# Kernel optimization log

Hardware: AMD Instinct MI355X
Metric: run time of the kernel (lower is better)

## Reference

```python
import jax, jax.numpy as jnp
import numpy as np

B, T, V, H, M = 32, 40, 64, 768, 64
U = 23            # number of never-visited vpids
N = 63            # total distinct vpids: visited 0..T-1, unvisited T..N-1
POS_D = 7         # angle_feat_size(4) + 3
MAX_STEPS = 100
TXT_L = 60
LN_EPS = 1e-12


def setup_inputs() -> dict:
    key = jax.random.key(0)
    ks = jax.random.split(key, 12)
    split_traj_embeds = jax.random.normal(ks[0], (B, T, V, H), jnp.float32)
    split_traj_vp_lens = jax.random.randint(ks[1], (B, T), 1, V + 1)
    traj_vpids = jnp.broadcast_to(jnp.arange(T, dtype=jnp.int32), (B, T))
    cand = jax.random.randint(ks[2], (B, T, V), 0, N).astype(jnp.int32)
    # guarantee every unvisited vpid (T..N-1) appears as a candidate at step 0
    cand = cand.at[:, 0, :U].set(jnp.broadcast_to(T + jnp.arange(U, dtype=jnp.int32), (B, U)))
    # gmap node 0 is the 'stop' token (feature forced to zero); nodes 1.. list all vpids
    gmap_vpids = jnp.broadcast_to(
        jnp.concatenate([jnp.zeros((1,), jnp.int32), jnp.arange(N, dtype=jnp.int32)]), (B, M))
    gmap_step_ids = jax.random.randint(ks[3], (B, M), 0, MAX_STEPS).astype(jnp.int32)
    gmap_pos_fts = jax.random.normal(ks[4], (B, M, POS_D), jnp.float32)
    gmap_lens = jax.random.randint(ks[5], (B,), M // 2, M + 1).astype(jnp.int32)
    txt_embeds = jax.random.normal(ks[6], (B, TXT_L, H), jnp.float32)
    txt_masks = jnp.ones((B, TXT_L), bool)
    # learned params
    W_pos = jax.random.normal(ks[7], (POS_D, H), jnp.float32) / np.sqrt(POS_D)
    b_pos = jnp.zeros((H,), jnp.float32)
    ln_gamma = jnp.ones((H,), jnp.float32)
    ln_beta = jnp.zeros((H,), jnp.float32)
    step_table = jax.random.normal(ks[8], (MAX_STEPS, H), jnp.float32) * 0.02
    return {
        'txt_embeds': txt_embeds, 'txt_masks': txt_masks,
        'split_traj_embeds': split_traj_embeds, 'split_traj_vp_lens': split_traj_vp_lens,
        'traj_vpids': traj_vpids, 'traj_cand_vpids': cand, 'gmap_vpids': gmap_vpids,
        'gmap_step_ids': gmap_step_ids, 'gmap_pos_fts': gmap_pos_fts, 'gmap_lens': gmap_lens,
        'W_pos': W_pos, 'b_pos': b_pos, 'ln_gamma': ln_gamma, 'ln_beta': ln_beta,
        'step_table': step_table,
    }


def _aggregate(split_traj_embeds, vp_lens, traj_vpids, traj_cand_vpids, gmap_vpids):
    dt = split_traj_embeds.dtype
    # mask out padded views, like split_traj_embeds * vp_masks
    view_mask = (jnp.arange(V) < vp_lens[:, :, None]).astype(dt)        # [B,T,V]
    emb_masked = split_traj_embeds * view_mask[..., None]               # [B,T,V,H]
    # per-step visited feature: sum over views / vp_len
    step_mean = emb_masked.sum(axis=2) / vp_lens[..., None].astype(dt)  # [B,T,H]
    # visited lookup: last step t with traj_vpids == gmap vpid
    visit_match = gmap_vpids[:, :, None] == traj_vpids[:, None, :]      # [B,M,T]
    visited = jnp.any(visit_match, axis=-1)                             # [B,M]
    last_t = jnp.argmax(jnp.where(visit_match, jnp.arange(T), -1), axis=-1)  # [B,M]
    visited_feat = step_mean[jnp.arange(B)[:, None], last_t]            # [B,M,H]
    # unvisited: mean of candidate-slot features over all (t, j) matches
    cand_match = (gmap_vpids[:, :, None, None] == traj_cand_vpids[:, None, :, :]).astype(dt)  # [B,M,T,V]
    unvis_sum = jnp.einsum('bmtv,btvh->bmh', cand_match, emb_masked)
    cnt = cand_match.sum(axis=(2, 3))                                   # [B,M]
    unvis_feat = unvis_sum / jnp.maximum(cnt, 1.0)[..., None]
    agg = jnp.where(visited[..., None], visited_feat, unvis_feat)       # [B,M,H]
    return agg.at[:, 0, :].set(0.0)  # stop-token slot is zeros


def _layernorm(x, gamma, beta):
    mu = x.mean(axis=-1, keepdims=True)
    var = ((x - mu) ** 2).mean(axis=-1, keepdims=True)
    return (x - mu) * jax.lax.rsqrt(var + LN_EPS) * gamma + beta


def reference(txt_embeds, txt_masks, split_traj_embeds, split_traj_vp_lens, traj_vpids,
              traj_cand_vpids, gmap_vpids, gmap_step_ids, gmap_pos_fts, gmap_lens,
              W_pos, b_pos, ln_gamma, ln_beta, step_table):
    agg = _aggregate(split_traj_embeds, split_traj_vp_lens, traj_vpids,
                     traj_cand_vpids, gmap_vpids)
    pos = _layernorm(gmap_pos_fts @ W_pos + b_pos, ln_gamma, ln_beta)   # [B,M,H]
    step = step_table[gmap_step_ids]                                    # [B,M,H]
    gmap_embeds = agg + step + pos
    return gmap_embeds
```

## Files before the change

kernel.cpp:

```cpp
#include <hip/hip_runtime.h>
#include <cstdint>

#define B 32
#define T 40
#define V 64
#define H 768
#define M 64
#define POS_D 7
#define NCODE 64
#define SEG 48
#define NBIN_BLKS (B * NCODE)
#define NSTEP (B * T)
#define NTAIL B

__device__ __forceinline__ void epilogue(
    int b, int m, float ax, float ay, float az, float aw,
    const float* __restrict__ pos_fts, const float* __restrict__ W_pos,
    const float* __restrict__ b_pos, const float* __restrict__ gamma,
    const float* __restrict__ beta, const int* __restrict__ step_ids,
    const float* __restrict__ step_tab, float* __restrict__ out,
    float* w1, float* w2)
{
    const int tid = threadIdx.x;
    const int hl = tid * 4;
    const int bm = b * M + m;

    float f[POS_D];
    #pragma unroll
    for (int d = 0; d < POS_D; ++d) f[d] = pos_fts[bm * POS_D + d];
    const float4 bp = *(const float4*)(b_pos + hl);
    float px = bp.x, py = bp.y, pz = bp.z, pw = bp.w;
    #pragma unroll
    for (int d = 0; d < POS_D; ++d) {
        const float4 wv4 = *(const float4*)(W_pos + d * H + hl);
        px += f[d] * wv4.x; py += f[d] * wv4.y;
        pz += f[d] * wv4.z; pw += f[d] * wv4.w;
    }

    float s1 = px + py + pz + pw;
    float s2 = px * px + py * py + pz * pz + pw * pw;
    #pragma unroll
    for (int off = 32; off > 0; off >>= 1) {
        s1 += __shfl_xor(s1, off);
        s2 += __shfl_xor(s2, off);
    }
    __syncthreads();
    const int wv = tid >> 6;
    if ((tid & 63) == 0) { w1[wv] = s1; w2[wv] = s2; }
    __syncthreads();
    s1 = w1[0] + w1[1] + w1[2];
    s2 = w2[0] + w2[1] + w2[2];
    const float mu = s1 * (1.0f / H);
    const float var = fmaxf(s2 * (1.0f / H) - mu * mu, 0.f);
    const float rs = rsqrtf(var + 1e-12f);

    const float4 gm = *(const float4*)(gamma + hl);
    const float4 bt4 = *(const float4*)(beta + hl);
    const int sid = step_ids[bm];
    const float4 st = *(const float4*)(step_tab + (size_t)sid * H + hl);

    float4 o;
    o.x = ax + st.x + (px - mu) * rs * gm.x + bt4.x;
    o.y = ay + st.y + (py - mu) * rs * gm.y + bt4.y;
    o.z = az + st.z + (pz - mu) * rs * gm.z + bt4.z;
    o.w = aw + st.w + (pw - mu) * rs * gm.w + bt4.w;
    *(float4*)(out + (size_t)bm * H + hl) = o;
}

__global__ __launch_bounds__(192) void fused_kernel(
    const float* __restrict__ emb, const int* __restrict__ lens,
    const int* __restrict__ cand, const int* __restrict__ tvp,
    const int* __restrict__ gvp, const int* __restrict__ step_ids,
    const float* __restrict__ pos_fts, const float* __restrict__ W_pos,
    const float* __restrict__ b_pos, const float* __restrict__ gamma,
    const float* __restrict__ beta, const float* __restrict__ step_tab,
    float* __restrict__ out)
{
    const int tid = threadIdx.x;
    const int blk = blockIdx.x;
    const int w = tid >> 6, lane = tid & 63;

    __shared__ int tvp_s[T], gvp_s[M], lens_s[T];
    __shared__ int code_s, cnt_s;
    __shared__ int list_s[3 * SEG];
    __shared__ int wcnt[3];
    __shared__ float w1[3], w2[3];

    if (blk < NBIN_BLKS) {
        const int b = blk >> 6, bin = blk & 63;

        if (tid < T) { tvp_s[tid] = tvp[b * T + tid]; lens_s[tid] = lens[b * T + tid]; }
        if (tid < M) gvp_s[tid] = gvp[b * M + tid];
        if (tid == 0) { code_s = -1; cnt_s = 0; }
        if (tid < 3) wcnt[tid] = 0;
        __syncthreads();

        if (tid < 64) {
            const int c = tid;
            bool mention = false;
            #pragma unroll 8
            for (int mm = 0; mm < M; ++mm) mention |= (gvp_s[mm] == c);
            bool vis = false;
            #pragma unroll 8
            for (int t = 0; t < T; ++t) vis |= (tvp_s[t] == c);
            const bool needed = mention && !vis;
            const unsigned long long mask = __ballot(needed);
            const int pre = __popcll(mask & ((1ull << c) - 1ull));
            if (needed && pre == bin) code_s = c;
        }
        __syncthreads();

        const int code = code_s;
        if (code < 0) return;

        const int* cb = cand + b * T * V;
        int local = 0;
        for (int i = tid; i < T * V; i += 192) local += (cb[i] == code);
        #pragma unroll
        for (int off = 32; off; off >>= 1) local += __shfl_xor(local, off);
        if (lane == 0) atomicAdd(&cnt_s, local);

        int myn = 0;
        for (int t = w; t < T; t += 3) {
            const int cc = cb[t * V + lane];
            const bool ok = (lane < lens_s[t]) && (cc == code);
            const unsigned long long mk = __ballot(ok);
            if (ok) {
                const int pos = myn + __popcll(mk & ((1ull << lane) - 1ull));
                if (pos < SEG) list_s[w * SEG + pos] = t * V + lane;
            }
            myn += __popcll(mk);
        }
        if (lane == 0) wcnt[w] = min(myn, SEG);
        __syncthreads();

        float ax = 0.f, ay = 0.f, az = 0.f, aw = 0.f;
        const float* eb = emb + (size_t)b * T * V * H + tid * 4;
        for (int ww = 0; ww < 3; ++ww) {
            const int n = wcnt[ww];
            #pragma unroll 8
            for (int k = 0; k < n; ++k) {
                const int tvx = list_s[ww * SEG + k];
                const float4 x = *(const float4*)(eb + (size_t)tvx * H);
                ax += x.x; ay += x.y; az += x.z; aw += x.w;
            }
        }
        const float inv = 1.0f / fmaxf((float)cnt_s, 1.0f);
        ax *= inv; ay *= inv; az *= inv; aw *= inv;

        for (int m = 1; m < M; ++m)
            if (gvp_s[m] == code)
                epilogue(b, m, ax, ay, az, aw, pos_fts, W_pos, b_pos,
                         gamma, beta, step_ids, step_tab, out, w1, w2);
        return;
    }

    if (blk < NBIN_BLKS + NSTEP) {
        const int bt = blk - NBIN_BLKS;
        const int b = bt / T, t = bt - b * T;

        if (tid < T) tvp_s[tid] = tvp[b * T + tid];
        if (tid < M) gvp_s[tid] = gvp[b * M + tid];
        __syncthreads();

        const int c = tvp_s[t];
        int lt = -1;
        #pragma unroll 8
        for (int tt = 0; tt < T; ++tt) if (tvp_s[tt] == c) lt = tt;
        if (lt != t) return;

        bool any = false;
        #pragma unroll 8
        for (int m = 1; m < M; ++m) any |= (gvp_s[m] == c);
        if (!any) return;

        const int len = lens[bt];
        const float* base = emb + (size_t)bt * V * H + tid * 4;
        float ax = 0.f, ay = 0.f, az = 0.f, aw = 0.f;
        int v = 0;
        for (; v + 16 <= len; v += 16) {
            #pragma unroll
            for (int u = 0; u < 16; ++u) {
                const float4 x = *(const float4*)(base + (size_t)(v + u) * H);
                ax += x.x; ay += x.y; az += x.z; aw += x.w;
            }
        }
        #pragma unroll 4
        for (; v < len; ++v) {
            const float4 x = *(const float4*)(base + (size_t)v * H);
            ax += x.x; ay += x.y; az += x.z; aw += x.w;
        }
        const float inv = 1.0f / (float)len;
        ax *= inv; ay *= inv; az *= inv; aw *= inv;

        for (int m = 1; m < M; ++m)
            if (gvp_s[m] == c)
                epilogue(b, m, ax, ay, az, aw, pos_fts, W_pos, b_pos,
                         gamma, beta, step_ids, step_tab, out, w1, w2);
        return;
    }

    {
        const int b = blk - (NBIN_BLKS + NSTEP);
        if (tid < M) gvp_s[tid] = gvp[b * M + tid];
        __syncthreads();
        for (int m = 0; m < M; ++m) {
            const int g = gvp_s[m];
            const bool handled = (m != 0) && (g >= 0) && (g < NCODE);
            if (!handled)
                epilogue(b, m, 0.f, 0.f, 0.f, 0.f, pos_fts, W_pos, b_pos,
                         gamma, beta, step_ids, step_tab, out, w1, w2);
        }
    }
}

extern "C" void kernel_launch(void* const* d_in, const int* in_sizes, int n_in,
                              void* d_out, int out_size, void* d_ws, size_t ws_size,
                              hipStream_t stream)
{
    const float* emb      = (const float*)d_in[2];
    const int*   vp_lens  = (const int*)d_in[3];
    const int*   tvp      = (const int*)d_in[4];
    const int*   cand     = (const int*)d_in[5];
    const int*   gvp      = (const int*)d_in[6];
    const int*   step_ids = (const int*)d_in[7];
    const float* pos_fts  = (const float*)d_in[8];
    const float* W_pos    = (const float*)d_in[10];
    const float* b_pos    = (const float*)d_in[11];
    const float* gamma    = (const float*)d_in[12];
    const float* beta     = (const float*)d_in[13];
    const float* step_tab = (const float*)d_in[14];
    float* out = (float*)d_out;

    fused_kernel<<<NBIN_BLKS + NSTEP + NTAIL, 192, 0, stream>>>(
        emb, vp_lens, cand, tvp, gvp, step_ids, pos_fts,
        W_pos, b_pos, gamma, beta, step_tab, out);
}
```

Before: 43.20 us.

## Double block size to split row reductions across two thread halves and reorder blocks

```diff
diff --git a/kernel.cpp b/kernel.cpp
--- a/kernel.cpp
+++ b/kernel.cpp
@@ -8,13 +8,15 @@
 #define M 64
 #define POS_D 7
 #define NCODE 64
-#define SEG 48
+#define THREADS 384
+#define SEGW 24
+#define NSTEP (B * T)
 #define NBIN_BLKS (B * NCODE)
-#define NSTEP (B * T)
 #define NTAIL B
 
 __device__ __forceinline__ void epilogue(
     int b, int m, float ax, float ay, float az, float aw,
+    bool act, int col4,
     const float* __restrict__ pos_fts, const float* __restrict__ W_pos,
     const float* __restrict__ b_pos, const float* __restrict__ gamma,
     const float* __restrict__ beta, const int* __restrict__ step_ids,
@@ -22,19 +24,22 @@
     float* w1, float* w2)
 {
     const int tid = threadIdx.x;
-    const int hl = tid * 4;
+    const int wv = tid >> 6, lane = tid & 63;
     const int bm = b * M + m;
 
-    float f[POS_D];
-    #pragma unroll
-    for (int d = 0; d < POS_D; ++d) f[d] = pos_fts[bm * POS_D + d];
-    const float4 bp = *(const float4*)(b_pos + hl);
-    float px = bp.x, py = bp.y, pz = bp.z, pw = bp.w;
-    #pragma unroll
-    for (int d = 0; d < POS_D; ++d) {
-        const float4 wv4 = *(const float4*)(W_pos + d * H + hl);
-        px += f[d] * wv4.x; py += f[d] * wv4.y;
-        pz += f[d] * wv4.z; pw += f[d] * wv4.w;
+    float px = 0.f, py = 0.f, pz = 0.f, pw = 0.f;
+    if (act) {
+        float f[POS_D];
+        #pragma unroll
+        for (int d = 0; d < POS_D; ++d) f[d] = pos_fts[bm * POS_D + d];
+        const float4 bp = *(const float4*)(b_pos + col4);
+        px = bp.x; py = bp.y; pz = bp.z; pw = bp.w;
+        #pragma unroll
+        for (int d = 0; d < POS_D; ++d) {
+            const float4 wv4 = *(const float4*)(W_pos + d * H + col4);
+            px += f[d] * wv4.x; py += f[d] * wv4.y;
+            pz += f[d] * wv4.z; pw += f[d] * wv4.w;
+        }
     }
 
     float s1 = px + py + pz + pw;
@@ -45,29 +50,29 @@
         s2 += __shfl_xor(s2, off);
     }
     __syncthreads();
-    const int wv = tid >> 6;
-    if ((tid & 63) == 0) { w1[wv] = s1; w2[wv] = s2; }
+    if (lane == 0) { w1[wv] = s1; w2[wv] = s2; }
     __syncthreads();
-    s1 = w1[0] + w1[1] + w1[2];
-    s2 = w2[0] + w2[1] + w2[2];
+    s1 = w1[0] + w1[1] + w1[2] + w1[3] + w1[4] + w1[5];
+    s2 = w2[0] + w2[1] + w2[2] + w2[3] + w2[4] + w2[5];
     const float mu = s1 * (1.0f / H);
     const float var = fmaxf(s2 * (1.0f / H) - mu * mu, 0.f);
     const float rs = rsqrtf(var + 1e-12f);
 
-    const float4 gm = *(const float4*)(gamma + hl);
-    const float4 bt4 = *(const float4*)(beta + hl);
-    const int sid = step_ids[bm];
-    const float4 st = *(const float4*)(step_tab + (size_t)sid * H + hl);
-
-    float4 o;
-    o.x = ax + st.x + (px - mu) * rs * gm.x + bt4.x;
-    o.y = ay + st.y + (py - mu) * rs * gm.y + bt4.y;
-    o.z = az + st.z + (pz - mu) * rs * gm.z + bt4.z;
-    o.w = aw + st.w + (pw - mu) * rs * gm.w + bt4.w;
-    *(float4*)(out + (size_t)bm * H + hl) = o;
+    if (act) {
+        const float4 gm = *(const float4*)(gamma + col4);
+        const float4 bt4 = *(const float4*)(beta + col4);
+        const int sid = step_ids[bm];
+        const float4 st = *(const float4*)(step_tab + (size_t)sid * H + col4);
+        float4 o;
+        o.x = ax + st.x + (px - mu) * rs * gm.x + bt4.x;
+        o.y = ay + st.y + (py - mu) * rs * gm.y + bt4.y;
+        o.z = az + st.z + (pz - mu) * rs * gm.z + bt4.z;
+        o.w = aw + st.w + (pw - mu) * rs * gm.w + bt4.w;
+        *(float4*)(out + (size_t)bm * H + col4) = o;
+    }
 }
 
-__global__ __launch_bounds__(192) void fused_kernel(
+__global__ __launch_bounds__(THREADS) void fused_kernel(
     const float* __restrict__ emb, const int* __restrict__ lens,
     const int* __restrict__ cand, const int* __restrict__ tvp,
     const int* __restrict__ gvp, const int* __restrict__ step_ids,
@@ -78,21 +83,92 @@
 {
     const int tid = threadIdx.x;
     const int blk = blockIdx.x;
-    const int w = tid >> 6, lane = tid & 63;
+    const int wv = tid >> 6, lane = tid & 63;
+    const bool act = tid < 192;
+    const int sub = act ? 0 : 1;
+    const int col4 = (act ? tid : tid - 192) * 4;
 
     __shared__ int tvp_s[T], gvp_s[M], lens_s[T];
     __shared__ int code_s, cnt_s;
-    __shared__ int list_s[3 * SEG];
-    __shared__ int wcnt[3];
-    __shared__ float w1[3], w2[3];
-
-    if (blk < NBIN_BLKS) {
-        const int b = blk >> 6, bin = blk & 63;
+    __shared__ int list_s[6 * SEGW];
+    __shared__ int wcnt[6];
+    __shared__ float comb[H];
+    __shared__ float w1[6], w2[6];
+
+    if (blk < NSTEP) {
+        const int bt = blk;
+        const int b = bt / T, t = bt - b * T;
+        if (tid < T) tvp_s[tid] = tvp[b * T + tid];
+        if (tid < M) gvp_s[tid] = gvp[b * M + tid];
+        __syncthreads();
+
+        const int c = tvp_s[t];
+        int lt = -1;
+        #pragma unroll 8
+        for (int tt = 0; tt < T; ++tt) if (tvp_s[tt] == c) lt = tt;
+        if (lt != t) return;
+        bool any = false;
+        #pragma unroll 8
+        for (int m = 1; m < M; ++m) any |= (gvp_s[m] == c);
+        if (!any) return;
+
+        const int len = lens[bt];
+        const float* base = emb + (size_t)bt * V * H + col4;
+        float ax = 0.f, ay = 0.f, az = 0.f, aw = 0.f;
+        int v = 0;
+        for (; v + 32 <= len; v += 32) {
+            #pragma unroll
+            for (int u = 0; u < 16; ++u) {
+                const float4 x = *(const float4*)(base + (size_t)(v + 2 * u + sub) * H);
+                ax += x.x; ay += x.y; az += x.z; aw += x.w;
+            }
+        }
+        for (; v + 16 <= len; v += 16) {
+            #pragma unroll
+            for (int u = 0; u < 8; ++u) {
+                const float4 x = *(const float4*)(base + (size_t)(v + 2 * u + sub) * H);
+                ax += x.x; ay += x.y; az += x.z; aw += x.w;
+            }
+        }
+        for (; v + 8 <= len; v += 8) {
+            #pragma unroll
+            for (int u = 0; u < 4; ++u) {
+                const float4 x = *(const float4*)(base + (size_t)(v + 2 * u + sub) * H);
+                ax += x.x; ay += x.y; az += x.z; aw += x.w;
+            }
+        }
+        for (; v + 2 <= len; v += 2) {
+            const float4 x = *(const float4*)(base + (size_t)(v + sub) * H);
+            ax += x.x; ay += x.y; az += x.z; aw += x.w;
+        }
+        if (v < len && sub == 0) {
+            const float4 x = *(const float4*)(base + (size_t)v * H);
+            ax += x.x; ay += x.y; az += x.z; aw += x.w;
+        }
+        if (!act) { float4 o; o.x = ax; o.y = ay; o.z = az; o.w = aw;
+                    *(float4*)(comb + col4) = o; }
+        __syncthreads();
+        if (act) {
+            const float4 o = *(const float4*)(comb + col4);
+            const float inv = 1.0f / (float)len;
+            ax = (ax + o.x) * inv; ay = (ay + o.y) * inv;
+            az = (az + o.z) * inv; aw = (aw + o.w) * inv;
+        }
+        for (int m = 1; m < M; ++m)
+            if (gvp_s[m] == c)
+                epilogue(b, m, ax, ay, az, aw, act, col4, pos_fts, W_pos, b_pos,
+                         gamma, beta, step_ids, step_tab, out, w1, w2);
+        return;
+    }
+
+    if (blk < NSTEP + NBIN_BLKS) {
+        const int bb = blk - NSTEP;
+        const int b = bb >> 6, bin = bb & 63;
 
         if (tid < T) { tvp_s[tid] = tvp[b * T + tid]; lens_s[tid] = lens[b * T + tid]; }
         if (tid < M) gvp_s[tid] = gvp[b * M + tid];
         if (tid == 0) { code_s = -1; cnt_s = 0; }
-        if (tid < 3) wcnt[tid] = 0;
+        if (tid < 6) wcnt[tid] = 0;
         __syncthreads();
 
         if (tid < 64) {
@@ -115,101 +191,61 @@
 
         const int* cb = cand + b * T * V;
         int local = 0;
-        for (int i = tid; i < T * V; i += 192) local += (cb[i] == code);
+        for (int i = tid; i < T * V; i += THREADS) local += (cb[i] == code);
         #pragma unroll
         for (int off = 32; off; off >>= 1) local += __shfl_xor(local, off);
         if (lane == 0) atomicAdd(&cnt_s, local);
 
         int myn = 0;
-        for (int t = w; t < T; t += 3) {
+        for (int t = wv; t < T; t += 6) {
             const int cc = cb[t * V + lane];
             const bool ok = (lane < lens_s[t]) && (cc == code);
             const unsigned long long mk = __ballot(ok);
             if (ok) {
                 const int pos = myn + __popcll(mk & ((1ull << lane) - 1ull));
-                if (pos < SEG) list_s[w * SEG + pos] = t * V + lane;
+                if (pos < SEGW) list_s[wv * SEGW + pos] = t * V + lane;
             }
             myn += __popcll(mk);
         }
-        if (lane == 0) wcnt[w] = min(myn, SEG);
+        if (lane == 0) wcnt[wv] = min(myn, SEGW);
         __syncthreads();
 
         float ax = 0.f, ay = 0.f, az = 0.f, aw = 0.f;
-        const float* eb = emb + (size_t)b * T * V * H + tid * 4;
-        for (int ww = 0; ww < 3; ++ww) {
+        const float* eb = emb + (size_t)b * T * V * H + col4;
+        for (int ww = 0; ww < 6; ++ww) {
             const int n = wcnt[ww];
-            #pragma unroll 8
-            for (int k = 0; k < n; ++k) {
-                const int tvx = list_s[ww * SEG + k];
-                const float4 x = *(const float4*)(eb + (size_t)tvx * H);
-                ax += x.x; ay += x.y; az += x.z; aw += x.w;
-            }
-        }
-        const float inv = 1.0f / fmaxf((float)cnt_s, 1.0f);
-        ax *= inv; ay *= inv; az *= inv; aw *= inv;
-
+            #pragma unroll 4
+            for (int k = sub; k < n; k += 2) {
+                const float4 x = *(const float4*)(eb + (size_t)list_s[ww * SEGW + k] * H);
+                ax += x.x; ay += x.y; az += x.z; aw += x.w;
+            }
+        }
+        if (!act) { float4 o; o.x = ax; o.y = ay; o.z = az; o.w = aw;
+                    *(float4*)(comb + col4) = o; }
+        __syncthreads();
+        if (act) {
+            const float4 o = *(const float4*)(comb + col4);
+            const float inv = 1.0f / fmaxf((float)cnt_s, 1.0f);
+            ax = (ax + o.x) * inv; ay = (ay + o.y) * inv;
+            az = (az + o.z) * inv; aw = (aw + o.w) * inv;
+        }
         for (int m = 1; m < M; ++m)
             if (gvp_s[m] == code)
-                epilogue(b, m, ax, ay, az, aw, pos_fts, W_pos, b_pos,
+                epilogue(b, m, ax, ay, az, aw, act, col4, pos_fts, W_pos, b_pos,
                          gamma, beta, step_ids, step_tab, out, w1, w2);
         return;
     }
 
-    if (blk < NBIN_BLKS + NSTEP) {
-        const int bt = blk - NBIN_BLKS;
-        const int b = bt / T, t = bt - b * T;
-
-        if (tid < T) tvp_s[tid] = tvp[b * T + tid];
-        if (tid < M) gvp_s[tid] = gvp[b * M + tid];
-        __syncthreads();
-
-        const int c = tvp_s[t];
-        int lt = -1;
-        #pragma unroll 8
-        for (int tt = 0; tt < T; ++tt) if (tvp_s[tt] == c) lt = tt;
-        if (lt != t) return;
-
-        bool any = false;
-        #pragma unroll 8
-        for (int m = 1; m < M; ++m) any |= (gvp_s[m] == c);
-        if (!any) return;
-
-        const int len = lens[bt];
-        const float* base = emb + (size_t)bt * V * H + tid * 4;
-        float ax = 0.f, ay = 0.f, az = 0.f, aw = 0.f;
-        int v = 0;
-        for (; v + 16 <= len; v += 16) {
-            #pragma unroll
-            for (int u = 0; u < 16; ++u) {
-                const float4 x = *(const float4*)(base + (size_t)(v + u) * H);
-                ax += x.x; ay += x.y; az += x.z; aw += x.w;
-            }
-        }
-        #pragma unroll 4
-        for (; v < len; ++v) {
-            const float4 x = *(const float4*)(base + (size_t)v * H);
-            ax += x.x; ay += x.y; az += x.z; aw += x.w;
-        }
-        const float inv = 1.0f / (float)len;
-        ax *= inv; ay *= inv; az *= inv; aw *= inv;
-
-        for (int m = 1; m < M; ++m)
-            if (gvp_s[m] == c)
-                epilogue(b, m, ax, ay, az, aw, pos_fts, W_pos, b_pos,
-                         gamma, beta, step_ids, step_tab, out, w1, w2);
-        return;
-    }
-
     {
-        const int b = blk - (NBIN_BLKS + NSTEP);
+        const int b = blk - (NSTEP + NBIN_BLKS);
         if (tid < M) gvp_s[tid] = gvp[b * M + tid];
         __syncthreads();
         for (int m = 0; m < M; ++m) {
             const int g = gvp_s[m];
             const bool handled = (m != 0) && (g >= 0) && (g < NCODE);
             if (!handled)
-                epilogue(b, m, 0.f, 0.f, 0.f, 0.f, pos_fts, W_pos, b_pos,
-                         gamma, beta, step_ids, step_tab, out, w1, w2);
+                epilogue(b, m, 0.f, 0.f, 0.f, 0.f, act, col4, pos_fts, W_pos,
+                         b_pos, gamma, beta, step_ids, step_tab, out, w1, w2);
         }
     }
 }
@@ -232,7 +268,7 @@
     const float* step_tab = (const float*)d_in[14];
     float* out = (float*)d_out;
 
-    fused_kernel<<<NBIN_BLKS + NSTEP + NTAIL, 192, 0, stream>>>(
+    fused_kernel<<<NSTEP + NBIN_BLKS + NTAIL, THREADS, 0, stream>>>(
         emb, vp_lens, cand, tvp, gvp, step_ids, pos_fts,
         W_pos, b_pos, gamma, beta, step_tab, out);
 }
```

New measurement: 77.99 us. 80.5% more time.

## Split work into independent wave-level tasks covering one third of H each

Applied to the files above, without the earlier changes.

```diff
diff --git a/kernel.cpp b/kernel.cpp
--- a/kernel.cpp
+++ b/kernel.cpp
@@ -8,66 +8,67 @@
 #define M 64
 #define POS_D 7
 #define NCODE 64
-#define SEG 48
-#define NBIN_BLKS (B * NCODE)
-#define NSTEP (B * T)
-#define NTAIL B
-
-__device__ __forceinline__ void epilogue(
-    int b, int m, float ax, float ay, float az, float aw,
+#define LCAP 96
+#define NBIN_WT (B * NCODE * 3)
+#define NSTEP_WT (B * T * 3)
+#define NCATCH_WT (B * 3)
+#define NWT (NBIN_WT + NSTEP_WT + NCATCH_WT)
+#define NBLK (NWT / 4)
+
+__device__ __forceinline__ void wave_epilogue(
+    int bm, int third, float ax, float ay, float az, float aw,
     const float* __restrict__ pos_fts, const float* __restrict__ W_pos,
     const float* __restrict__ b_pos, const float* __restrict__ gamma,
     const float* __restrict__ beta, const int* __restrict__ step_ids,
-    const float* __restrict__ step_tab, float* __restrict__ out,
-    float* w1, float* w2)
+    const float* __restrict__ step_tab, float* __restrict__ out)
 {
-    const int tid = threadIdx.x;
-    const int hl = tid * 4;
-    const int bm = b * M + m;
+    const int lane = threadIdx.x & 63;
 
     float f[POS_D];
     #pragma unroll
     for (int d = 0; d < POS_D; ++d) f[d] = pos_fts[bm * POS_D + d];
-    const float4 bp = *(const float4*)(b_pos + hl);
-    float px = bp.x, py = bp.y, pz = bp.z, pw = bp.w;
+
+    float s1 = 0.f, s2 = 0.f;
+    float kx = 0.f, ky = 0.f, kz = 0.f, kw = 0.f;
     #pragma unroll
-    for (int d = 0; d < POS_D; ++d) {
-        const float4 wv4 = *(const float4*)(W_pos + d * H + hl);
-        px += f[d] * wv4.x; py += f[d] * wv4.y;
-        pz += f[d] * wv4.z; pw += f[d] * wv4.w;
-    }
-
-    float s1 = px + py + pz + pw;
-    float s2 = px * px + py * py + pz * pz + pw * pw;
+    for (int g = 0; g < 3; ++g) {
+        const int c0 = g * 256 + lane * 4;
+        const float4 bp = *(const float4*)(b_pos + c0);
+        float px = bp.x, py = bp.y, pz = bp.z, pw = bp.w;
+        #pragma unroll
+        for (int d = 0; d < POS_D; ++d) {
+            const float4 wv = *(const float4*)(W_pos + d * H + c0);
+            px += f[d] * wv.x; py += f[d] * wv.y;
+            pz += f[d] * wv.z; pw += f[d] * wv.w;
+        }
+        s1 += px + py + pz + pw;
+        s2 += px * px + py * py + pz * pz + pw * pw;
+        if (g == third) { kx = px; ky = py; kz = pz; kw = pw; }
+    }
     #pragma unroll
     for (int off = 32; off > 0; off >>= 1) {
         s1 += __shfl_xor(s1, off);
         s2 += __shfl_xor(s2, off);
     }
-    __syncthreads();
-    const int wv = tid >> 6;
-    if ((tid & 63) == 0) { w1[wv] = s1; w2[wv] = s2; }
-    __syncthreads();
-    s1 = w1[0] + w1[1] + w1[2];
-    s2 = w2[0] + w2[1] + w2[2];
     const float mu = s1 * (1.0f / H);
     const float var = fmaxf(s2 * (1.0f / H) - mu * mu, 0.f);
     const float rs = rsqrtf(var + 1e-12f);
 
-    const float4 gm = *(const float4*)(gamma + hl);
-    const float4 bt4 = *(const float4*)(beta + hl);
+    const int oc = third * 256 + lane * 4;
+    const float4 gm = *(const float4*)(gamma + oc);
+    const float4 bt = *(const float4*)(beta + oc);
     const int sid = step_ids[bm];
-    const float4 st = *(const float4*)(step_tab + (size_t)sid * H + hl);
+    const float4 st = *(const float4*)(step_tab + (size_t)sid * H + oc);
 
     float4 o;
-    o.x = ax + st.x + (px - mu) * rs * gm.x + bt4.x;
-    o.y = ay + st.y + (py - mu) * rs * gm.y + bt4.y;
-    o.z = az + st.z + (pz - mu) * rs * gm.z + bt4.z;
-    o.w = aw + st.w + (pw - mu) * rs * gm.w + bt4.w;
-    *(float4*)(out + (size_t)bm * H + hl) = o;
+    o.x = ax + st.x + (kx - mu) * rs * gm.x + bt.x;
+    o.y = ay + st.y + (ky - mu) * rs * gm.y + bt.y;
+    o.z = az + st.z + (kz - mu) * rs * gm.z + bt.z;
+    o.w = aw + st.w + (kw - mu) * rs * gm.w + bt.w;
+    *(float4*)(out + (size_t)bm * H + oc) = o;
 }
 
-__global__ __launch_bounds__(192) void fused_kernel(
+__global__ __launch_bounds__(256) void fused_kernel(
     const float* __restrict__ emb, const int* __restrict__ lens,
     const int* __restrict__ cand, const int* __restrict__ tvp,
     const int* __restrict__ gvp, const int* __restrict__ step_ids,
@@ -77,105 +78,102 @@
     float* __restrict__ out)
 {
     const int tid = threadIdx.x;
-    const int blk = blockIdx.x;
     const int w = tid >> 6, lane = tid & 63;
-
-    __shared__ int tvp_s[T], gvp_s[M], lens_s[T];
-    __shared__ int code_s, cnt_s;
-    __shared__ int list_s[3 * SEG];
-    __shared__ int wcnt[3];
-    __shared__ float w1[3], w2[3];
-
-    if (blk < NBIN_BLKS) {
-        const int b = blk >> 6, bin = blk & 63;
-
-        if (tid < T) { tvp_s[tid] = tvp[b * T + tid]; lens_s[tid] = lens[b * T + tid]; }
-        if (tid < M) gvp_s[tid] = gvp[b * M + tid];
-        if (tid == 0) { code_s = -1; cnt_s = 0; }
-        if (tid < 3) wcnt[tid] = 0;
-        __syncthreads();
-
-        if (tid < 64) {
-            const int c = tid;
-            bool mention = false;
-            #pragma unroll 8
-            for (int mm = 0; mm < M; ++mm) mention |= (gvp_s[mm] == c);
-            bool vis = false;
-            #pragma unroll 8
-            for (int t = 0; t < T; ++t) vis |= (tvp_s[t] == c);
-            const bool needed = mention && !vis;
-            const unsigned long long mask = __ballot(needed);
-            const int pre = __popcll(mask & ((1ull << c) - 1ull));
-            if (needed && pre == bin) code_s = c;
-        }
-        __syncthreads();
-
-        const int code = code_s;
-        if (code < 0) return;
+    const int wt = blockIdx.x * 4 + w;
+
+    __shared__ int list_all[4][LCAP];
+    int* list = list_all[w];
+
+    if (wt < NBIN_WT) {
+        const int b = wt / (NCODE * 3);
+        const int r = wt - b * (NCODE * 3);
+        const int bin = r / 3, third = r - bin * 3;
+
+        const int gv = (lane < M) ? gvp[b * M + lane] : -1;
+        const int tv = (lane < T) ? tvp[b * T + lane] : -1;
+        const int ln = (lane < T) ? lens[b * T + lane] : 0;
+
+        unsigned long long mentioned =
+            (lane > 0 && gv >= 0 && gv < NCODE) ? (1ull << gv) : 0ull;
+        unsigned long long visited =
+            (lane < T && tv >= 0 && tv < NCODE) ? (1ull << tv) : 0ull;
+        #pragma unroll
+        for (int off = 32; off > 0; off >>= 1) {
+            mentioned |= __shfl_xor(mentioned, off);
+            visited   |= __shfl_xor(visited, off);
+        }
+        const unsigned long long needed = mentioned & ~visited;
+
+        const bool mine = ((needed >> lane) & 1ull) &&
+            (__popcll(needed & ((1ull << lane) - 1ull)) == bin);
+        const unsigned long long mm = __ballot(mine);
+        if (mm == 0ull) return;
+        const int code = __ffsll((unsigned long long)mm) - 1;
 
         const int* cb = cand + b * T * V;
-        int local = 0;
-        for (int i = tid; i < T * V; i += 192) local += (cb[i] == code);
-        #pragma unroll
-        for (int off = 32; off; off >>= 1) local += __shfl_xor(local, off);
-        if (lane == 0) atomicAdd(&cnt_s, local);
-
-        int myn = 0;
-        for (int t = w; t < T; t += 3) {
-            const int cc = cb[t * V + lane];
-            const bool ok = (lane < lens_s[t]) && (cc == code);
-            const unsigned long long mk = __ballot(ok);
+        int cnt = 0, myn = 0;
+        #pragma unroll 4
+        for (int t = 0; t < T; ++t) {
+            const int cv = cb[t * V + lane];
+            const bool eq = (cv == code);
+            cnt += __popcll(__ballot(eq));
+            const int len_t = __shfl(ln, t);
+            const bool ok = eq && (lane < len_t);
+            const unsigned long long mok = __ballot(ok);
             if (ok) {
-                const int pos = myn + __popcll(mk & ((1ull << lane) - 1ull));
-                if (pos < SEG) list_s[w * SEG + pos] = t * V + lane;
-            }
-            myn += __popcll(mk);
-        }
-        if (lane == 0) wcnt[w] = min(myn, SEG);
-        __syncthreads();
-
+                const int pos = myn + __popcll(mok & ((1ull << lane) - 1ull));
+                if (pos < LCAP) list[pos] = t * V + lane;
+            }
+            myn += __popcll(mok);
+        }
+        const int n = min(myn, LCAP);
+
+        const float* eb = emb + (size_t)b * T * V * H + third * 256 + lane * 4;
         float ax = 0.f, ay = 0.f, az = 0.f, aw = 0.f;
-        const float* eb = emb + (size_t)b * T * V * H + tid * 4;
-        for (int ww = 0; ww < 3; ++ww) {
-            const int n = wcnt[ww];
-            #pragma unroll 8
-            for (int k = 0; k < n; ++k) {
-                const int tvx = list_s[ww * SEG + k];
-                const float4 x = *(const float4*)(eb + (size_t)tvx * H);
+        int k = 0;
+        for (; k + 8 <= n; k += 8) {
+            #pragma unroll
+            for (int u = 0; u < 8; ++u) {
+                const float4 x = *(const float4*)(eb + (size_t)list[k + u] * H);
                 ax += x.x; ay += x.y; az += x.z; aw += x.w;
             }
         }
-        const float inv = 1.0f / fmaxf((float)cnt_s, 1.0f);
+        for (; k < n; ++k) {
+            const float4 x = *(const float4*)(eb + (size_t)list[k] * H);
+            ax += x.x; ay += x.y; az += x.z; aw += x.w;
+        }
+        const float inv = 1.0f / fmaxf((float)cnt, 1.0f);
         ax *= inv; ay *= inv; az *= inv; aw *= inv;
 
-        for (int m = 1; m < M; ++m)
-            if (gvp_s[m] == code)
-                epilogue(b, m, ax, ay, az, aw, pos_fts, W_pos, b_pos,
-                         gamma, beta, step_ids, step_tab, out, w1, w2);
+        unsigned long long cm = __ballot(lane > 0 && gv == code);
+        while (cm) {
+            const int m = __ffsll(cm) - 1;
+            wave_epilogue(b * M + m, third, ax, ay, az, aw, pos_fts, W_pos,
+                          b_pos, gamma, beta, step_ids, step_tab, out);
+            cm &= cm - 1ull;
+        }
         return;
     }
 
-    if (blk < NBIN_BLKS + NSTEP) {
-        const int bt = blk - NBIN_BLKS;
-        const int b = bt / T, t = bt - b * T;
-
-        if (tid < T) tvp_s[tid] = tvp[b * T + tid];
-        if (tid < M) gvp_s[tid] = gvp[b * M + tid];
-        __syncthreads();
-
-        const int c = tvp_s[t];
-        int lt = -1;
-        #pragma unroll 8
-        for (int tt = 0; tt < T; ++tt) if (tvp_s[tt] == c) lt = tt;
+    if (wt < NBIN_WT + NSTEP_WT) {
+        const int q = wt - NBIN_WT;
+        const int b = q / (T * 3);
+        const int r = q - b * (T * 3);
+        const int t = r / 3, third = r - t * 3;
+
+        const int gv = (lane < M) ? gvp[b * M + lane] : -1;
+        const int tv = (lane < T) ? tvp[b * T + lane] : -2147483647;
+
+        const int c = __shfl(tv, t);
+        const unsigned long long meq = __ballot(lane < T && tv == c);
+        const int lt = 63 - __clzll(meq);
         if (lt != t) return;
-
-        bool any = false;
-        #pragma unroll 8
-        for (int m = 1; m < M; ++m) any |= (gvp_s[m] == c);
-        if (!any) return;
-
-        const int len = lens[bt];
-        const float* base = emb + (size_t)bt * V * H + tid * 4;
+        const unsigned long long cm0 = __ballot(lane > 0 && gv == c);
+        if (cm0 == 0ull) return;
+
+        const int len = lens[b * T + t];
+        const float* base = emb + ((size_t)(b * T + t)) * V * H
+                            + third * 256 + lane * 4;
         float ax = 0.f, ay = 0.f, az = 0.f, aw = 0.f;
         int v = 0;
         for (; v + 16 <= len; v += 16) {
@@ -185,7 +183,13 @@
                 ax += x.x; ay += x.y; az += x.z; aw += x.w;
             }
         }
-        #pragma unroll 4
+        for (; v + 4 <= len; v += 4) {
+            #pragma unroll
+            for (int u = 0; u < 4; ++u) {
+                const float4 x = *(const float4*)(base + (size_t)(v + u) * H);
+                ax += x.x; ay += x.y; az += x.z; aw += x.w;
+            }
+        }
         for (; v < len; ++v) {
             const float4 x = *(const float4*)(base + (size_t)v * H);
             ax += x.x; ay += x.y; az += x.z; aw += x.w;
@@ -193,23 +197,27 @@
         const float inv = 1.0f / (float)len;
         ax *= inv; ay *= inv; az *= inv; aw *= inv;
 
-        for (int m = 1; m < M; ++m)
-            if (gvp_s[m] == c)
-                epilogue(b, m, ax, ay, az, aw, pos_fts, W_pos, b_pos,
-                         gamma, beta, step_ids, step_tab, out, w1, w2);
+        unsigned long long cm = cm0;
+        while (cm) {
+            const int m = __ffsll(cm) - 1;
+            wave_epilogue(b * M + m, third, ax, ay, az, aw, pos_fts, W_pos,
+                          b_pos, gamma, beta, step_ids, step_tab, out);
+            cm &= cm - 1ull;
+        }
         return;
     }
 
     {
-        const int b = blk - (NBIN_BLKS + NSTEP);
-        if (tid < M) gvp_s[tid] = gvp[b * M + tid];
-        __syncthreads();
-        for (int m = 0; m < M; ++m) {
-            const int g = gvp_s[m];
-            const bool handled = (m != 0) && (g >= 0) && (g < NCODE);
-            if (!handled)
-                epilogue(b, m, 0.f, 0.f, 0.f, 0.f, pos_fts, W_pos, b_pos,
-                         gamma, beta, step_ids, step_tab, out, w1, w2);
+        const int q = wt - (NBIN_WT + NSTEP_WT);
+        const int b = q / 3, third = q - (q / 3) * 3;
+        const int gv = (lane < M) ? gvp[b * M + lane] : 0;
+        unsigned long long um =
+            __ballot(lane == 0 || gv < 0 || gv >= NCODE);
+        while (um) {
+            const int m = __ffsll(um) - 1;
+            wave_epilogue(b * M + m, third, 0.f, 0.f, 0.f, 0.f, pos_fts, W_pos,
+                          b_pos, gamma, beta, step_ids, step_tab, out);
+            um &= um - 1ull;
         }
     }
 }
@@ -232,7 +240,7 @@
     const float* step_tab = (const float*)d_in[14];
     float* out = (float*)d_out;
 
-    fused_kernel<<<NBIN_BLKS + NSTEP + NTAIL, 192, 0, stream>>>(
+    fused_kernel<<<NBLK, 256, 0, stream>>>(
         emb, vp_lens, cand, tvp, gvp, step_ids, pos_fts,
         W_pos, b_pos, gamma, beta, step_tab, out);
 }
```

New measurement: 48.74 us. 12.8% more time.
